# Kernel tuning notes

Measured on AMD Instinct MI355X. Metric: run time of the kernel, lower is better.

## Reference

```python
import jax, jax.numpy as jnp
import numpy as np

SCALE = 2
K_UP = 5
K_ENC = 3


def _conv(x, w, b, pad):
    # NCHW conv, OIHW weights
    y = jax.lax.conv_general_dilated(
        x, w, window_strides=(1, 1), padding=((pad, pad), (pad, pad)),
        dimension_numbers=('NCHW', 'OIHW', 'NCHW'))
    return y + b[None, :, None, None]


def setup_inputs() -> dict:
    key = jax.random.key(0)
    k0, k1, k2 = jax.random.split(key, 3)
    b, c, h, w = 4, 256, 64, 64
    c_mid = 64
    n_kernel = SCALE * SCALE * K_UP * K_UP  # 100
    x = jax.random.normal(k0, (b, c, h, w), jnp.float32)
    w1 = jax.random.normal(k1, (c_mid, c, K_ENC, K_ENC), jnp.float32) * 0.02
    b1 = jnp.zeros((c_mid,), jnp.float32)
    w2 = jax.random.normal(k2, (n_kernel, c_mid, 1, 1), jnp.float32) * 0.02
    b2 = jnp.zeros((n_kernel,), jnp.float32)
    return {"x": x, "w1": w1, "b1": b1, "w2": w2, "b2": b2}


def reference(x, w1, b1, w2, b2):
    b, c, h, w = x.shape
    s, k = SCALE, K_UP
    # kernel prediction encoder: 3x3 conv -> ReLU -> 1x1 conv
    feat = jax.nn.relu(_conv(x, w1, b1, K_ENC // 2))
    kern = _conv(feat, w2, b2, 0)                     # (b, s^2*k^2, h, w)
    kern = jax.nn.softmax(kern, axis=1)               # softmax over full channel dim (as in source)
    kern = kern.reshape(b, s * s, k * k, h, w)
    # F.unfold(x, k, padding=k//2) -> (b, c, k^2, h, w); torch ordering: kh major, kw minor
    pad = k // 2
    xp = jnp.pad(x, ((0, 0), (0, 0), (pad, pad), (pad, pad)))
    patches = jnp.stack([xp[:, :, i:i + h, j:j + w]
                         for i in range(k) for j in range(k)], axis=2)  # (b, c, k^2, h, w)
    # per-pixel weighted reassembly: sum over k^2 neighborhood
    out = jnp.einsum('bskhw,bckhw->bschw', kern, patches)  # (b, s^2, c, h, w)
    # view(b, s^2*c, h, w) then pixel_shuffle(scale), exactly matching torch semantics
    out = out.reshape(b, s * s * c, h, w)
    cout = (s * s * c) // (s * s)
    out = out.reshape(b, cout, s, s, h, w)
    out = out.transpose(0, 1, 4, 2, 5, 3).reshape(b, cout, h * s, w * s)
    return out
```

## Files before the change

### kernel.cpp

```cpp
#include <hip/hip_runtime.h>


#define BB 4
#define CC 256
#define HH 64
#define WW 64
#define CMID 64
#define NKCH 100

typedef __bf16 bf16;
typedef __bf16 bf16x8 __attribute__((ext_vector_type(8)));
typedef float f32x4 __attribute__((ext_vector_type(4)));

__device__ __forceinline__ void async_copy16(const void* gsrc, void* ldst) {
    __builtin_amdgcn_global_load_lds(
        (__attribute__((address_space(1))) void*)(void*)gsrc,
        (__attribute__((address_space(3))) void*)ldst, 16, 0, 0);
}

__global__ void k0a_transform(const float* __restrict__ w1, const float* __restrict__ w2,
                              bf16* __restrict__ w1c, bf16* __restrict__ w2c) {
    int c8 = blockIdx.x;
    int oq = blockIdx.y;
    int tid = threadIdx.x;
    __shared__ __align__(16) float wf[16 * 300];

    for (int i = tid; i < 16 * 72; i += 256) {
        int o = i / 72, r = i % 72;
        *(float4*)&wf[o * 300 + r * 4] =
            *(const float4*)&w1[(size_t)(oq * 16 + o) * 2304 + c8 * 288 + r * 4];
    }
    __syncthreads();

    for (int t = tid; t < 576; t += 256) {
        int o = t & 15, q = (t >> 4) & 3, kk = t >> 6;
        union { bf16 h[8]; uint4 u; } v;
        #pragma unroll
        for (int i8 = 0; i8 < 8; ++i8)
            v.h[i8] = (bf16)wf[o * 300 + (q * 8 + i8) * 9 + kk];
        *(uint4*)&w1c[(size_t)((((c8 * 9 + kk) * 4 + q) * 64) + oq * 16 + o) * 8] = v.u;
    }

    if (c8 == 0 && oq == 0) {
        for (int i = tid; i < 7168; i += 256) {
            int i8 = i & 7;
            int oc = (i >> 3) % 112;
            int kq = (i >> 3) / 112;
            int ic = (kq >> 2) * 32 + (kq & 3) * 8 + i8;
            w2c[i] = (oc < NKCH) ? (bf16)w2[oc * 64 + ic] : (bf16)0.f;
        }
    }
}

__global__ __launch_bounds__(512) void k123_fused(const float* __restrict__ x,
        const bf16* __restrict__ w1c, const bf16* __restrict__ w2c,
        const float* __restrict__ b1, const float* __restrict__ b2,
        float* __restrict__ out) {
    int bh = blockIdx.x;
    int b = bh >> 6, h = bh & 63;
    int tid = threadIdx.x;
    int lane = tid & 63, wid = tid >> 6;
    int l15 = lane & 15, quad = lane >> 4;
    int mhalf = wid & 1, nq = wid >> 1;

    __shared__ __align__(16) char smem[115968];
    bf16*  xs0  = (bf16*)smem;
    bf16*  xs1  = (bf16*)(smem + 15872);
    bf16*  wl0  = (bf16*)(smem + 31744);
    bf16*  wl1  = (bf16*)(smem + 68608);
    bf16*  fsb  = (bf16*)(smem + 105472);
    float* ls   = (float*)(smem + 31744);
    float* kts  = (float*)(smem + 68608);
    float* red  = (float*)smem;

    const float* xb = x + (size_t)b * (CC * HH * WW);

    int ppp[6], rrr[6];
    bool vmask[6];
    #pragma unroll
    for (int j = 0; j < 6; ++j) {
        int task = wid + j * 8;
        ppp[j] = task & 15;
        rrr[j] = task >> 4;
        int hr = h - 1 + rrr[j];
        vmask[j] = (hr >= 0 && hr < HH);
    }

    float fA0[6], fA1[6], fB0[6], fB1[6];
    #define LOADX(C8, F0, F1)                                                    \
        _Pragma("unroll")                                                        \
        for (int j = 0; j < 6; ++j) {                                            \
            if (vmask[j]) {                                                      \
                const float* src = xb + ((size_t)((C8) * 32 + 2 * ppp[j]) * (HH * WW)) \
                                 + (h - 1 + rrr[j]) * WW + lane;                 \
                F0[j] = src[0]; F1[j] = src[HH * WW];                            \
            }                                                                    \
        }
    #define WRITEB(F0, F1, XSDST)                                                \
        _Pragma("unroll")                                                        \
        for (int j = 0; j < 6; ++j) {                                            \
            if (vmask[j]) {                                                      \
                union { bf16 hh[2]; unsigned u; } cv;                            \
                cv.hh[0] = (bf16)F0[j]; cv.hh[1] = (bf16)F1[j];                  \
                *(unsigned*)&(XSDST)[(rrr[j] * 66 + 1 + lane) * 40 + 2 * ppp[j]] = cv.u; \
            }                                                                    \
        }
    #define ACOPY(C8, WDST)                                                      \
        for (int t = wid; t < 36; t += 8)                                        \
            async_copy16(w1c + ((((C8) * 36 + t) << 9) + lane * 8), (void*)&(WDST)[t << 9]);
    #define MFMAS(XSRC, WSRC)                                                    \
        _Pragma("unroll")                                                        \
        for (int kk = 0; kk < 9; ++kk) {                                         \
            int r3 = kk / 3, kw = kk % 3;                                        \
            bf16x8 a0 = *(const bf16x8*)&(WSRC)[((kk * 4 + quad) * 64 + mhalf * 32 + l15) * 8]; \
            bf16x8 a1 = *(const bf16x8*)&(WSRC)[((kk * 4 + quad) * 64 + mhalf * 32 + 16 + l15) * 8]; \
            bf16x8 xv = *(const bf16x8*)&(XSRC)[(r3 * 66 + nq * 16 + l15 + kw) * 40 + quad * 8]; \
            acc0 = __builtin_amdgcn_mfma_f32_16x16x32_bf16(a0, xv, acc0, 0, 0, 0); \
            acc1 = __builtin_amdgcn_mfma_f32_16x16x32_bf16(a1, xv, acc1, 0, 0, 0); \
        }

    for (int i = tid; i < 7936; i += 512) { xs0[i] = (bf16)0.f; xs1[i] = (bf16)0.f; }
    LOADX(0, fA0, fA1)
    ACOPY(0, wl0)
    __syncthreads();
    WRITEB(fA0, fA1, xs0)
    LOADX(1, fB0, fB1)
    __syncthreads();

    f32x4 acc0 = {0.f, 0.f, 0.f, 0.f}, acc1 = {0.f, 0.f, 0.f, 0.f};

    for (int c8 = 0; c8 < 8; c8 += 2) {
        ACOPY(c8 + 1, wl1)
        if (c8 < 6) { LOADX(c8 + 2, fA0, fA1) }
        MFMAS(xs0, wl0)
        WRITEB(fB0, fB1, xs1)
        __syncthreads();
        if (c8 < 6) { ACOPY(c8 + 2, wl0) }
        if (c8 < 6) { LOADX(c8 + 3, fB0, fB1) }
        MFMAS(xs1, wl1)
        if (c8 < 6) { WRITEB(fA0, fA1, xs0) }
        __syncthreads();
    }

    int px = nq * 16 + l15;
    #pragma unroll
    for (int mi = 0; mi < 2; ++mi) {
        int oc0 = mhalf * 32 + mi * 16 + quad * 4;
        float4 bv = *(const float4*)&b1[oc0];
        f32x4 v = mi ? acc1 : acc0;
        union { bf16 hh[4]; unsigned long long u; } o;
        o.hh[0] = (bf16)fmaxf(v[0] + bv.x, 0.f);
        o.hh[1] = (bf16)fmaxf(v[1] + bv.y, 0.f);
        o.hh[2] = (bf16)fmaxf(v[2] + bv.z, 0.f);
        o.hh[3] = (bf16)fmaxf(v[3] + bv.w, 0.f);
        *(unsigned long long*)&fsb[px * 72 + oc0] = o.u;
    }
    __syncthreads();

    int t8 = tid & 255, h2 = tid >> 8;
    int w3 = t8 & 63, cg3 = t8 >> 6;
    #define XLOAD(P, V)                                                          \
        _Pragma("unroll")                                                        \
        for (int k = 0; k < 5; ++k) {                                            \
            int idx = t8 + k * 256;                                              \
            int u = idx & 15, cc = (idx >> 4) & 15, rr = idx >> 8;               \
            int hr = h - 2 + rr;                                                 \
            V[k] = make_float4(0.f, 0.f, 0.f, 0.f);                              \
            if (hr >= 0 && hr < HH)                                              \
                V[k] = *(const float4*)&x[(((size_t)b * CC + (2 * (P) + h2) * 16 + cc) * HH + hr) * WW + 4 * u]; \
        }
    #define XWRITE(V, TB)                                                        \
        _Pragma("unroll")                                                        \
        for (int k = 0; k < 5; ++k) {                                            \
            int idx = t8 + k * 256;                                              \
            int u = idx & 15, cc = (idx >> 4) & 15, rr = idx >> 8;               \
            int bse = (rr * 4 + (cc >> 2)) * 68;                                 \
            int c = cc & 3;                                                      \
            _Pragma("unroll")                                                    \
            for (int j = 0; j < 4; ++j) {                                        \
                int s = 2 + 4 * u + j;                                           \
                int sw = s ^ ((s >> 3) & 7);                                     \
                (TB)[(bse + sw) * 4 + c] = ((const float*)&V[k])[j];             \
            }                                                                    \
        }
    float4 xst[5];
    XLOAD(0, xst)

    if (wid < 7) {
        f32x4 lacc0 = {0.f,0.f,0.f,0.f}, lacc1 = {0.f,0.f,0.f,0.f};
        f32x4 lacc2 = {0.f,0.f,0.f,0.f}, lacc3 = {0.f,0.f,0.f,0.f};
        #pragma unroll
        for (int kk = 0; kk < 2; ++kk) {
            bf16x8 a = *(const bf16x8*)&w2c[(((kk * 4 + quad) * 112) + wid * 16 + l15) * 8];
            bf16x8 bf0 = *(const bf16x8*)&fsb[( 0 + l15) * 72 + kk * 32 + quad * 8];
            bf16x8 bf1 = *(const bf16x8*)&fsb[(16 + l15) * 72 + kk * 32 + quad * 8];
            bf16x8 bf2 = *(const bf16x8*)&fsb[(32 + l15) * 72 + kk * 32 + quad * 8];
            bf16x8 bf3 = *(const bf16x8*)&fsb[(48 + l15) * 72 + kk * 32 + quad * 8];
            lacc0 = __builtin_amdgcn_mfma_f32_16x16x32_bf16(a, bf0, lacc0, 0, 0, 0);
            lacc1 = __builtin_amdgcn_mfma_f32_16x16x32_bf16(a, bf1, lacc1, 0, 0, 0);
            lacc2 = __builtin_amdgcn_mfma_f32_16x16x32_bf16(a, bf2, lacc2, 0, 0, 0);
            lacc3 = __builtin_amdgcn_mfma_f32_16x16x32_bf16(a, bf3, lacc3, 0, 0, 0);
        }
        f32x4 laccs[4] = {lacc0, lacc1, lacc2, lacc3};
        #pragma unroll
        for (int nt = 0; nt < 4; ++nt)
            #pragma unroll
            for (int j = 0; j < 4; ++j) {
                int oc = wid * 16 + quad * 4 + j;
                if (oc < NKCH) ls[oc * 64 + nt * 16 + l15] = laccs[nt][j];
            }
    }
    __syncthreads();

    int w = lane;
    int g = wid, s2 = g & 3, ihalf = g >> 2;
    int i0 = ihalf ? 13 : 0;

    float lg[13];
    #pragma unroll
    for (int ii = 0; ii < 13; ++ii) {
        int idx = i0 + ii;
        bool act = (idx < 25);
        int oc = s2 * 25 + (act ? idx : 0);
        lg[ii] = act ? (ls[oc * 64 + w] + b2[oc]) : -1e30f;
    }

    float m = -1e30f;
    #pragma unroll
    for (int ii = 0; ii < 13; ++ii) m = fmaxf(m, lg[ii]);
    red[g * 64 + w] = m;
    __syncthreads();
    m = fmaxf(fmaxf(fmaxf(red[0 * 64 + w], red[1 * 64 + w]),
                    fmaxf(red[2 * 64 + w], red[3 * 64 + w])),
              fmaxf(fmaxf(red[4 * 64 + w], red[5 * 64 + w]),
                    fmaxf(red[6 * 64 + w], red[7 * 64 + w])));
    float ssum = 0.f;
    #pragma unroll
    for (int ii = 0; ii < 13; ++ii) { lg[ii] = __expf(lg[ii] - m); ssum += lg[ii]; }
    red[512 + g * 64 + w] = ssum;
    __syncthreads();
    ssum = ((red[512 + 0 * 64 + w] + red[512 + 1 * 64 + w]) +
            (red[512 + 2 * 64 + w] + red[512 + 3 * 64 + w])) +
           ((red[512 + 4 * 64 + w] + red[512 + 5 * 64 + w]) +
            (red[512 + 6 * 64 + w] + red[512 + 7 * 64 + w]));
    float inv = 1.f / ssum;
    #pragma unroll
    for (int ii = 0; ii < 13; ++ii)
        if (i0 + ii < 25) kts[((i0 + ii) * 64 + w) * 4 + s2] = lg[ii] * inv;
    __syncthreads();

    #pragma unroll
    for (int reg = 0; reg < 4; ++reg) {
        const int tb = (reg == 0) ? 0 : (reg == 1) ? 21760 : (reg == 2) ? 43520 : 94208;
        if (tid < 320) {
            int c = tid & 3, q = (tid >> 2) & 3, rg = tid >> 4;
            int slot = (q < 2) ? q : (q + 64);
            ((float*)(smem + tb))[(rg * 68 + slot) * 4 + c] = 0.f;
        }
    }

    float* tb0 = (float*)(smem + (h2 ? 21760 : 0));
    float* tb1 = (float*)(smem + (h2 ? 94208 : 43520));

    int swk[5];
    #pragma unroll
    for (int kw = 0; kw < 5; ++kw) {
        int s = w3 + kw;
        swk[kw] = s ^ ((s >> 3) & 7);
    }

    XWRITE(xst, tb0)
    __syncthreads();

    for (int p = 0; p < 8; ++p) {
        if (p < 7) { XLOAD(p + 1, xst) }
        float* T = (p & 1) ? tb1 : tb0;
        f32x4 a0 = {0.f,0.f,0.f,0.f}, a1 = {0.f,0.f,0.f,0.f};
        f32x4 a2 = {0.f,0.f,0.f,0.f}, a3 = {0.f,0.f,0.f,0.f};
        #pragma unroll
        for (int r = 0; r < 5; ++r) {
            #pragma unroll
            for (int kw = 0; kw < 5; ++kw) {
                f32x4 kvv = *(const f32x4*)&kts[((r * 5 + kw) * 64 + w3) * 4];
                f32x4 xv = *(const f32x4*)&T[((r * 4 + cg3) * 68 + swk[kw]) * 4];
                a0 += kvv.x * xv;
                a1 += kvv.y * xv;
                a2 += kvv.z * xv;
                a3 += kvv.w * xv;
            }
        }
        int cq = (2 * p + h2) * 4 + cg3;
        f32x4 accs[4] = {a0, a1, a2, a3};
        #pragma unroll
        for (int s = 0; s < 4; ++s) {
            size_t base = (((size_t)b * 256 + s * 64 + cq) * 128 + 2 * h) * 128 + 2 * w3;
            *(float2*)&out[base]       = make_float2(accs[s][0], accs[s][1]);
            *(float2*)&out[base + 128] = make_float2(accs[s][2], accs[s][3]);
        }
        if (p < 7) {
            float* Tnext = (p & 1) ? tb0 : tb1;
            XWRITE(xst, Tnext)
        }
        __syncthreads();
    }
    #undef LOADX
    #undef WRITEB
    #undef ACOPY
    #undef MFMAS
    #undef XLOAD
    #undef XWRITE
}

extern "C" void kernel_launch(void* const* d_in, const int* in_sizes, int n_in,
                              void* d_out, int out_size, void* d_ws, size_t ws_size,
                              hipStream_t stream) {
    const float* x  = (const float*)d_in[0];
    const float* w1 = (const float*)d_in[1];
    const float* b1 = (const float*)d_in[2];
    const float* w2 = (const float*)d_in[3];
    const float* b2 = (const float*)d_in[4];
    float* out = (float*)d_out;

    char* wsb = (char*)d_ws;
    bf16* w1c = (bf16*)wsb;
    bf16* w2c = (bf16*)(wsb + 294912);

    k0a_transform<<<dim3(8, 4), 256, 0, stream>>>(w1, w2, w1c, w2c);
    k123_fused<<<dim3(BB * HH), 512, 0, stream>>>(x, w1c, w2c, b1, b2, out);
}
```

Measured before the change: 122.7 us.

## Restructure conv x-tile staging to channel-group layout with 16-byte LDS writes

Changes the shared-memory layout of the bf16 input tile from a padded row-major stride-40 layout to a [row][channel-group][pixel][8] layout. Each thread now loads 8 channels and writes one 16-byte vector, instead of many 4-byte writes. The stage buffers shrink, and the later-phase tile buffers are moved to new offsets within a larger LDS allocation. It also replaces several __syncthreads with a raw lgkmcnt wait plus s_barrier, which skips waiting on outstanding global memory ops. That carries a risk if any of those ops must complete before the barrier.

New measurement: 121.9 us. No clear change (-0.6%).

```diff
diff --git a/kernel.cpp b/kernel.cpp
--- a/kernel.cpp
+++ b/kernel.cpp
@@ -11,6 +11,8 @@
 typedef __bf16 bf16;
 typedef __bf16 bf16x8 __attribute__((ext_vector_type(8)));
 typedef float f32x4 __attribute__((ext_vector_type(4)));
+
+#define BAR_LGKM() asm volatile("s_waitcnt lgkmcnt(0)\n\ts_barrier" ::: "memory")
 
 __device__ __forceinline__ void async_copy16(const void* gsrc, void* ldst) {
     __builtin_amdgcn_global_load_lds(
@@ -63,82 +65,90 @@
     int l15 = lane & 15, quad = lane >> 4;
     int mhalf = wid & 1, nq = wid >> 1;
 
-    __shared__ __align__(16) char smem[115968];
+    __shared__ __align__(16) char smem[131584];
     bf16*  xs0  = (bf16*)smem;
-    bf16*  xs1  = (bf16*)(smem + 15872);
-    bf16*  wl0  = (bf16*)(smem + 31744);
-    bf16*  wl1  = (bf16*)(smem + 68608);
-    bf16*  fsb  = (bf16*)(smem + 105472);
-    float* ls   = (float*)(smem + 31744);
-    float* kts  = (float*)(smem + 68608);
+    bf16*  xs1  = (bf16*)(smem + 12800);
+    bf16*  wl0  = (bf16*)(smem + 25600);
+    bf16*  wl1  = (bf16*)(smem + 62464);
+    bf16*  fsb  = (bf16*)(smem + 99328);
+    float* ls   = (float*)(smem + 25600);
+    float* kts  = (float*)(smem + 62464);
     float* red  = (float*)smem;
 
     const float* xb = x + (size_t)b * (CC * HH * WW);
 
-    int ppp[6], rrr[6];
-    bool vmask[6];
-    #pragma unroll
-    for (int j = 0; j < 6; ++j) {
-        int task = wid + j * 8;
-        ppp[j] = task & 15;
-        rrr[j] = task >> 4;
-        int hr = h - 1 + rrr[j];
-        vmask[j] = (hr >= 0 && hr < HH);
-    }
-
-    float fA0[6], fA1[6], fB0[6], fB1[6];
-    #define LOADX(C8, F0, F1)                                                    \
-        _Pragma("unroll")                                                        \
-        for (int j = 0; j < 6; ++j) {                                            \
-            if (vmask[j]) {                                                      \
-                const float* src = xb + ((size_t)((C8) * 32 + 2 * ppp[j]) * (HH * WW)) \
-                                 + (h - 1 + rrr[j]) * WW + lane;                 \
-                F0[j] = src[0]; F1[j] = src[HH * WW];                            \
-            }                                                                    \
-        }
-    #define WRITEB(F0, F1, XSDST)                                                \
-        _Pragma("unroll")                                                        \
-        for (int j = 0; j < 6; ++j) {                                            \
-            if (vmask[j]) {                                                      \
-                union { bf16 hh[2]; unsigned u; } cv;                            \
-                cv.hh[0] = (bf16)F0[j]; cv.hh[1] = (bf16)F1[j];                  \
-                *(unsigned*)&(XSDST)[(rrr[j] * 66 + 1 + lane) * 40 + 2 * ppp[j]] = cv.u; \
-            }                                                                    \
-        }
-    #define ACOPY(C8, WDST)                                                      \
-        for (int t = wid; t < 36; t += 8)                                        \
+    int g0 = wid & 3, r0 = wid >> 2;
+    bool tv1 = (wid < 4);
+    int hr0 = h - 1 + r0;
+    int hr1 = h + 1;
+    bool vm0 = (hr0 >= 0 && hr0 < HH);
+    bool vm1 = (hr1 < HH);
+
+    float fA[16], fB[16];
+    #define LOADX(C8, F)                                                          \
+        {                                                                         \
+            if (vm0) {                                                            \
+                const float* s0 = xb + ((size_t)((C8) * 32 + g0 * 8) * (HH * WW)) \
+                                 + hr0 * WW + lane;                               \
+                _Pragma("unroll")                                                 \
+                for (int i = 0; i < 8; ++i) F[i] = s0[(size_t)i * (HH * WW)];     \
+            }                                                                     \
+            if (tv1 && vm1) {                                                     \
+                const float* s1 = xb + ((size_t)((C8) * 32 + g0 * 8) * (HH * WW)) \
+                                 + hr1 * WW + lane;                               \
+                _Pragma("unroll")                                                 \
+                for (int i = 0; i < 8; ++i) F[8 + i] = s1[(size_t)i * (HH * WW)]; \
+            }                                                                     \
+        }
+    #define WRITEB(F, XSDST)                                                      \
+        {                                                                         \
+            if (vm0) {                                                            \
+                union { bf16 hh[8]; uint4 u; } cv;                                \
+                _Pragma("unroll")                                                 \
+                for (int i = 0; i < 8; ++i) cv.hh[i] = (bf16)F[i];                \
+                *(uint4*)&(XSDST)[((r0 * 4 + g0) * 66 + 1 + lane) * 8] = cv.u;    \
+            }                                                                     \
+            if (tv1 && vm1) {                                                     \
+                union { bf16 hh[8]; uint4 u; } cv;                                \
+                _Pragma("unroll")                                                 \
+                for (int i = 0; i < 8; ++i) cv.hh[i] = (bf16)F[8 + i];            \
+                *(uint4*)&(XSDST)[((2 * 4 + g0) * 66 + 1 + lane) * 8] = cv.u;     \
+            }                                                                     \
+        }
+    #define ACOPY(C8, WDST)                                                       \
+        for (int t = wid; t < 36; t += 8)                                         \
             async_copy16(w1c + ((((C8) * 36 + t) << 9) + lane * 8), (void*)&(WDST)[t << 9]);
-    #define MFMAS(XSRC, WSRC)                                                    \
-        _Pragma("unroll")                                                        \
-        for (int kk = 0; kk < 9; ++kk) {                                         \
-            int r3 = kk / 3, kw = kk % 3;                                        \
+    #define MFMAS(XSRC, WSRC)                                                     \
+        _Pragma("unroll")                                                         \
+        for (int kk = 0; kk < 9; ++kk) {                                          \
+            int r3 = kk / 3, kw = kk % 3;                                         \
             bf16x8 a0 = *(const bf16x8*)&(WSRC)[((kk * 4 + quad) * 64 + mhalf * 32 + l15) * 8]; \
             bf16x8 a1 = *(const bf16x8*)&(WSRC)[((kk * 4 + quad) * 64 + mhalf * 32 + 16 + l15) * 8]; \
-            bf16x8 xv = *(const bf16x8*)&(XSRC)[(r3 * 66 + nq * 16 + l15 + kw) * 40 + quad * 8]; \
+            bf16x8 xv = *(const bf16x8*)&(XSRC)[((r3 * 4 + quad) * 66 + nq * 16 + l15 + kw) * 8]; \
             acc0 = __builtin_amdgcn_mfma_f32_16x16x32_bf16(a0, xv, acc0, 0, 0, 0); \
             acc1 = __builtin_amdgcn_mfma_f32_16x16x32_bf16(a1, xv, acc1, 0, 0, 0); \
         }
 
-    for (int i = tid; i < 7936; i += 512) { xs0[i] = (bf16)0.f; xs1[i] = (bf16)0.f; }
-    LOADX(0, fA0, fA1)
+    for (int i = tid; i < 6336; i += 512) { xs0[i] = (bf16)0.f; xs1[i] = (bf16)0.f; }
+    LOADX(0, fA)
     ACOPY(0, wl0)
     __syncthreads();
-    WRITEB(fA0, fA1, xs0)
-    LOADX(1, fB0, fB1)
+    WRITEB(fA, xs0)
+    LOADX(1, fB)
     __syncthreads();
 
     f32x4 acc0 = {0.f, 0.f, 0.f, 0.f}, acc1 = {0.f, 0.f, 0.f, 0.f};
 
     for (int c8 = 0; c8 < 8; c8 += 2) {
         ACOPY(c8 + 1, wl1)
-        if (c8 < 6) { LOADX(c8 + 2, fA0, fA1) }
+        if (c8 < 6) { LOADX(c8 + 2, fA) }
         MFMAS(xs0, wl0)
-        WRITEB(fB0, fB1, xs1)
+        WRITEB(fB, xs1)
         __syncthreads();
         if (c8 < 6) { ACOPY(c8 + 2, wl0) }
-        if (c8 < 6) { LOADX(c8 + 3, fB0, fB1) }
+        if (c8 < 6) { LOADX(c8 + 3, fB) }
         MFMAS(xs1, wl1)
-        if (c8 < 6) { WRITEB(fA0, fA1, xs0) }
+        if (c8 < 6) { WRITEB(fA, xs0) }
         __syncthreads();
     }
 
@@ -210,7 +220,7 @@
                 if (oc < NKCH) ls[oc * 64 + nt * 16 + l15] = laccs[nt][j];
             }
     }
-    __syncthreads();
+    BAR_LGKM();
 
     int w = lane;
     int g = wid, s2 = g & 3, ihalf = g >> 2;
@@ -229,7 +239,7 @@
     #pragma unroll
     for (int ii = 0; ii < 13; ++ii) m = fmaxf(m, lg[ii]);
     red[g * 64 + w] = m;
-    __syncthreads();
+    BAR_LGKM();
     m = fmaxf(fmaxf(fmaxf(red[0 * 64 + w], red[1 * 64 + w]),
                     fmaxf(red[2 * 64 + w], red[3 * 64 + w])),
               fmaxf(fmaxf(red[4 * 64 + w], red[5 * 64 + w]),
@@ -238,7 +248,7 @@
     #pragma unroll
     for (int ii = 0; ii < 13; ++ii) { lg[ii] = __expf(lg[ii] - m); ssum += lg[ii]; }
     red[512 + g * 64 + w] = ssum;
-    __syncthreads();
+    BAR_LGKM();
     ssum = ((red[512 + 0 * 64 + w] + red[512 + 1 * 64 + w]) +
             (red[512 + 2 * 64 + w] + red[512 + 3 * 64 + w])) +
            ((red[512 + 4 * 64 + w] + red[512 + 5 * 64 + w]) +
@@ -247,11 +257,11 @@
     #pragma unroll
     for (int ii = 0; ii < 13; ++ii)
         if (i0 + ii < 25) kts[((i0 + ii) * 64 + w) * 4 + s2] = lg[ii] * inv;
-    __syncthreads();
+    BAR_LGKM();
 
     #pragma unroll
     for (int reg = 0; reg < 4; ++reg) {
-        const int tb = (reg == 0) ? 0 : (reg == 1) ? 21760 : (reg == 2) ? 43520 : 94208;
+        const int tb = (reg == 0) ? 0 : (reg == 1) ? 21760 : (reg == 2) ? 88064 : 109824;
         if (tid < 320) {
             int c = tid & 3, q = (tid >> 2) & 3, rg = tid >> 4;
             int slot = (q < 2) ? q : (q + 64);
@@ -260,7 +270,7 @@
     }
 
     float* tb0 = (float*)(smem + (h2 ? 21760 : 0));
-    float* tb1 = (float*)(smem + (h2 ? 94208 : 43520));
+    float* tb1 = (float*)(smem + (h2 ? 109824 : 88064));
 
     int swk[5];
     #pragma unroll
@@ -270,7 +280,7 @@
     }
 
     XWRITE(xst, tb0)
-    __syncthreads();
+    BAR_LGKM();
 
     for (int p = 0; p < 8; ++p) {
         if (p < 7) { XLOAD(p + 1, xst) }
@@ -301,7 +311,7 @@
             float* Tnext = (p & 1) ? tb0 : tb1;
             XWRITE(xst, Tnext)
         }
-        __syncthreads();
+        BAR_LGKM();
     }
     #undef LOADX
     #undef WRITEB
```
